# Kernel optimization log

Measured on AMD Instinct MI355X. Metric: run time of the kernel, lower is better.

The kernel has to match this reference:

```python
import jax, jax.numpy as jnp
import numpy as np

B, S, E, H = 8, 2048, 1024, 4
D = E // H  # per-head attention embed_dim (torch MHA with num_heads=1)


def setup_inputs() -> dict:
    key = jax.random.key(0)
    ks = jax.random.split(key, 7)
    scale = 0.02
    return {
        "x": jax.random.normal(ks[0], (B, S, E), dtype=jnp.float32),
        # outer linear: torch Linear(E, E) -> y = x @ W.T + b
        "W_lin": jax.random.normal(ks[1], (E, E), dtype=jnp.float32) * scale,
        "b_lin": jnp.zeros((E,), dtype=jnp.float32),
        # per-head MultiheadAttention params, stacked over H heads
        # in_proj: [3D, D] weight, [3D] bias per head (q,k,v stacked)
        "W_in": jax.random.normal(ks[2], (H, 3 * D, D), dtype=jnp.float32) * scale,
        "b_in": jnp.zeros((H, 3 * D), dtype=jnp.float32),
        # out_proj: [D, D] weight, [D] bias per head
        "W_out": jax.random.normal(ks[3], (H, D, D), dtype=jnp.float32) * scale,
        "b_out": jnp.zeros((H, D), dtype=jnp.float32),
    }


def _forward(x, W_lin, b_lin, W_in, b_in, W_out, b_out):
    # outer projection
    x_proj = jnp.einsum("bse,fe->bsf", x, W_lin) + b_lin          # [B,S,E]
    # torch.chunk(dim=-1) into H contiguous slices of width D == reshape
    xs = x_proj.reshape(B, S, H, D)                                 # [B,S,H,D]
    # per-head in_proj (q,k,v share input; weights stacked as [3D, D])
    qkv = jnp.einsum("bshd,hed->bshe", xs, W_in) + b_in             # [B,S,H,3D]
    q, k, v = jnp.split(qkv, 3, axis=-1)                            # each [B,S,H,D]
    # scaled dot-product attention per head (inner num_heads=1 -> head dim D)
    scores = jnp.einsum("bshd,bthd->bhst", q, k) / jnp.sqrt(jnp.float32(D))
    attn = jax.nn.softmax(scores, axis=-1)                          # [B,H,S,S]
    out = jnp.einsum("bhst,bthd->bshd", attn, v)                    # [B,S,H,D]
    # per-head out_proj
    out = jnp.einsum("bshd,hed->bshe", out, W_out) + b_out          # [B,S,H,D]
    # concat heads back along feature dim
    return out.reshape(B, S, E)


def reference(x, W_lin, b_lin, W_in, b_in, W_out, b_out):
    return _forward(x, W_lin, b_lin, W_in, b_in, W_out, b_out)
```

## Files before the change

### kernel.cpp

```cpp
#include <hip/hip_runtime.h>


typedef unsigned short u16;
typedef short s8v __attribute__((ext_vector_type(8)));
typedef float f4v __attribute__((ext_vector_type(4)));
typedef unsigned short us8v __attribute__((ext_vector_type(8)));

typedef const __attribute__((address_space(1))) void* gas_t;
typedef __attribute__((address_space(3))) void* las_t;

#define QSCALE 0.09016844f

__device__ __forceinline__ u16 f2bf(float f) {
  unsigned u = __builtin_bit_cast(unsigned, f);
  unsigned r = u + 0x7FFFu + ((u >> 16) & 1u);
  return (u16)(r >> 16);
}

__device__ __forceinline__ unsigned cvtpk(float a, float b) {
  unsigned r;
  asm("v_cvt_pk_bf16_f32 %0, %1, %2" : "=v"(r) : "v"(a), "v"(b));
  return r;
}

__device__ __forceinline__ void gload16(const void* g, void* l) {
  __builtin_amdgcn_global_load_lds((gas_t)g, (las_t)l, 16, 0, 0);
}

__global__ void cast_all(const float* __restrict__ x, const float* __restrict__ Wl,
                         const float* __restrict__ Wi, const float* __restrict__ Wo,
                         u16* __restrict__ xb, u16* __restrict__ WLb,
                         u16* __restrict__ WIb, u16* __restrict__ WOb) {
  const int i = blockIdx.x * blockDim.x + threadIdx.x;
  const float* src;
  u16* dst;
  int j;
  float sc = 1.0f;
  if (i < 4194304) {
    src = x; dst = xb; j = i;
  } else {
    const int k = i - 4194304;
    if (k < 262144) {
      src = Wl; dst = WLb; j = k;
    } else if (k < 458752) {
      src = Wi; dst = WIb; j = k - 262144;
      if (((j >> 6) % 768) < 256) sc = QSCALE;
    } else {
      src = Wo; dst = WOb; j = k - 458752;
    }
  }
  const float4 v = reinterpret_cast<const float4*>(src)[j];
  ushort4 o;
  o.x = f2bf(v.x * sc); o.y = f2bf(v.y * sc); o.z = f2bf(v.z * sc); o.w = f2bf(v.w * sc);
  reinterpret_cast<ushort4*>(dst)[j] = o;
}

template <int MODE>
__global__ void __launch_bounds__(256, 2) gemm128(
    const u16* __restrict__ A, const u16* __restrict__ Bw,
    const float* __restrict__ bias,
    u16* __restrict__ outB, float* __restrict__ outF,
    u16* __restrict__ Qo, u16* __restrict__ Ko, u16* __restrict__ Vo)
{
  constexpr int K    = (MODE == 0) ? 1024 : 256;
  constexpr int LDA  = 1024;
  constexpr int LDB  = (MODE == 0) ? 1024 : 256;
  constexpr int SMEM = (MODE == 1) ? 35072 : 32768;

  const int bx = blockIdx.x, ny = blockIdx.y, h = blockIdx.z;
  const int tid = threadIdx.x;
  const int wid = tid >> 6, l = tid & 63;
  const int l15 = l & 15, lg = l >> 4;
  const int wr = wid >> 1, wc = wid & 1;

  __shared__ __align__(16) char smem[SMEM];
  char* Al = smem;
  char* Bl = smem + 16384;

  const u16* Abase = A + (size_t)bx * 128 * LDA + ((MODE == 0) ? 0 : h * 256);
  const size_t bwoff = (MODE == 0) ? 0
                      : ((MODE == 1) ? (size_t)h * 768 * 256 : (size_t)h * 256 * 256);
  const u16* Bbase = Bw + bwoff + (size_t)ny * 128 * LDB;

  f4v acc[4][4];
#pragma unroll
  for (int i = 0; i < 4; ++i)
#pragma unroll
    for (int j = 0; j < 4; ++j) acc[i][j] = f4v{0.f, 0.f, 0.f, 0.f};

  for (int k0 = 0; k0 < K; k0 += 64) {
    __syncthreads();
#pragma unroll
    for (int ii = 0; ii < 4; ++ii) {
      const int i = wid * 4 + ii;
      const int row = i * 8 + (l >> 3);
      const int c = l & 7;
      gload16(Abase + (size_t)row * LDA + k0 + ((c ^ (row & 7)) << 3), Al + i * 1024);
    }
#pragma unroll
    for (int ii = 0; ii < 4; ++ii) {
      const int i = wid * 4 + ii;
      const int row = i * 8 + (l >> 3);
      const int c = l & 7;
      gload16(Bbase + (size_t)row * LDB + k0 + ((c ^ (row & 7)) << 3), Bl + i * 1024);
    }
    __syncthreads();
#pragma unroll
    for (int kf = 0; kf < 2; ++kf) {
      s8v a[4];
#pragma unroll
      for (int mf = 0; mf < 4; ++mf) {
        const int row = wr * 64 + mf * 16 + l15;
        a[mf] = *reinterpret_cast<const s8v*>(
            Al + row * 128 + (((kf * 32 + lg * 8) << 1) ^ ((row & 7) << 4)));
      }
#pragma unroll
      for (int nf = 0; nf < 4; ++nf) {
        const int n = wc * 64 + nf * 16 + l15;
        const s8v b = *reinterpret_cast<const s8v*>(
            Bl + n * 128 + (((kf * 32 + lg * 8) << 1) ^ ((n & 7) << 4)));
#pragma unroll
        for (int mf = 0; mf < 4; ++mf)
          acc[mf][nf] = __builtin_amdgcn_mfma_f32_16x16x32_bf16(a[mf], b, acc[mf][nf], 0, 0, 0);
      }
    }
  }

  const int mbase = bx * 128 + wr * 64;
  const int nbase = ny * 128 + wc * 64;

  if constexpr (MODE == 0) {
#pragma unroll
    for (int nf = 0; nf < 4; ++nf) {
      const int colg = nbase + nf * 16 + l15;
      const float bv = bias[colg];
#pragma unroll
      for (int mf = 0; mf < 4; ++mf)
#pragma unroll
        for (int r = 0; r < 4; ++r) {
          const int mr = mbase + mf * 16 + lg * 4 + r;
          outB[(size_t)mr * 1024 + colg] = f2bf(acc[mf][nf][r] + bv);
        }
    }
  } else if constexpr (MODE == 2) {
#pragma unroll
    for (int nf = 0; nf < 4; ++nf) {
      const int colg = nbase + nf * 16 + l15;
      const float bv = bias[h * 256 + colg];
#pragma unroll
      for (int mf = 0; mf < 4; ++mf)
#pragma unroll
        for (int r = 0; r < 4; ++r) {
          const int mr = mbase + mf * 16 + lg * 4 + r;
          outF[(size_t)mr * 1024 + h * 256 + colg] = acc[mf][nf][r] + bv;
        }
    }
  } else {
    if (ny < 4) {
      u16* dst = (ny < 2) ? Qo : Ko;
      const int cb = (ny < 2) ? 0 : 256;
#pragma unroll
      for (int nf = 0; nf < 4; ++nf) {
        const int colg = nbase + nf * 16 + l15;
        const float bscale = (ny < 2) ? QSCALE : 1.0f;
        const float bv = bias[h * 768 + colg] * bscale;
        const int d = colg - cb;
#pragma unroll
        for (int mf = 0; mf < 4; ++mf)
#pragma unroll
          for (int r = 0; r < 4; ++r) {
            const int mr = mbase + mf * 16 + lg * 4 + r;
            const int b = mr >> 11, s = mr & 2047;
            dst[((size_t)(b * 4 + h) * 2048 + s) * 256 + d] = f2bf(acc[mf][nf][r] + bv);
          }
      }
    } else {
      __syncthreads();
      short* tr = reinterpret_cast<short*>(smem);
#pragma unroll
      for (int nf = 0; nf < 4; ++nf) {
        const int colg = nbase + nf * 16 + l15;
        const float bv = bias[h * 768 + colg];
        const int cl = wc * 64 + nf * 16 + l15;
#pragma unroll
        for (int mf = 0; mf < 4; ++mf)
#pragma unroll
          for (int r = 0; r < 4; ++r) {
            const int rl = wr * 64 + mf * 16 + lg * 4 + r;
            tr[rl * 137 + cl] = (short)f2bf(acc[mf][nf][r] + bv);
          }
      }
      __syncthreads();
      const int b = bx >> 4;
#pragma unroll
      for (int rep = 0; rep < 8; ++rep) {
        const int u = rep * 256 + tid;
        const int d = u >> 4, sb = u & 15;
        const int dglob = (ny - 4) * 128 + d;
        const int tile = (bx & 15) * 2 + (sb >> 3);
        const int c = sb & 7;
        const int kA = 32 * (c >> 2) + 8 * ((2 * c) & 3) + 4 * ((c >> 1) & 1);
        u16* base = Vo + (((size_t)(b * 4 + h) * 32 + tile) * 256 + dglob) * 64;
        ushort4 lo, hi;
        lo.x = (u16)tr[(sb * 8 + 0) * 137 + d];
        lo.y = (u16)tr[(sb * 8 + 1) * 137 + d];
        lo.z = (u16)tr[(sb * 8 + 2) * 137 + d];
        lo.w = (u16)tr[(sb * 8 + 3) * 137 + d];
        hi.x = (u16)tr[(sb * 8 + 4) * 137 + d];
        hi.y = (u16)tr[(sb * 8 + 5) * 137 + d];
        hi.z = (u16)tr[(sb * 8 + 6) * 137 + d];
        hi.w = (u16)tr[(sb * 8 + 7) * 137 + d];
        *reinterpret_cast<ushort4*>(base + kA)     = lo;
        *reinterpret_cast<ushort4*>(base + kA + 8) = hi;
      }
    }
  }
}

__global__ void __launch_bounds__(256, 2) attn_fwd(
    const u16* __restrict__ Q, const u16* __restrict__ Kk,
    const u16* __restrict__ Vt, u16* __restrict__ AO)
{
  const int qt = blockIdx.x;
  const int bh = blockIdx.y;
  const int tid = threadIdx.x;
  const int wid = tid >> 6, l = tid & 63;
  const int l15 = l & 15, lg = l >> 4;

  __shared__ __align__(16) char smem[65536];
  char* Kl = smem;
  char* Vl = smem + 32768;

  const size_t kbase = (size_t)bh * 2048 * 256;

  s8v qa[8];
  {
    const u16* qrow = Q + ((size_t)bh * 2048 + qt * 64 + wid * 16 + l15) * 256;
#pragma unroll
    for (int kf = 0; kf < 8; ++kf)
      qa[kf] = *reinterpret_cast<const s8v*>(qrow + kf * 32 + lg * 8);
  }

  f4v O[16];
#pragma unroll
  for (int df = 0; df < 16; ++df) O[df] = f4v{0.f, 0.f, 0.f, 0.f};
  float m_run = -1e30f, l_run = 0.f;

  for (int t0 = 0; t0 < 2048; t0 += 64) {
    __syncthreads();
#pragma unroll
    for (int ii = 0; ii < 8; ++ii) {
      const int i = wid * 8 + ii;
      const int row = i * 2 + (l >> 5);
      const int c = l & 31;
      gload16(Kk + kbase + (size_t)(t0 + row) * 256 + ((c ^ (row & 7)) << 3), Kl + i * 1024);
    }
    {
      const u16* vtile = Vt + ((size_t)bh * 32 + (t0 >> 6)) * 16384;
#pragma unroll
      for (int ii = 0; ii < 8; ++ii) {
        const int i = wid * 8 + ii;
        const int d = i * 8 + (l >> 3);
        const int c = l & 7;
        gload16(vtile + (size_t)d * 64 + ((c ^ (d & 7)) << 3), Vl + i * 1024);
      }
    }
    __syncthreads();

    f4v Sx[4];
#pragma unroll
    for (int nf = 0; nf < 4; ++nf) Sx[nf] = f4v{0.f, 0.f, 0.f, 0.f};
#pragma unroll
    for (int kf = 0; kf < 8; ++kf) {
      const int ch = kf * 4 + lg;
#pragma unroll
      for (int nf = 0; nf < 4; ++nf) {
        const int tl = nf * 16 + l15;
        const s8v kb = *reinterpret_cast<const s8v*>(
            Kl + tl * 512 + ((ch ^ (tl & 7)) << 4));
        Sx[nf] = __builtin_amdgcn_mfma_f32_16x16x32_bf16(kb, qa[kf], Sx[nf], 0, 0, 0);
      }
    }

    float mloc = fmaxf(fmaxf(fmaxf(Sx[0][0], Sx[0][1]), fmaxf(Sx[0][2], Sx[0][3])),
                       fmaxf(fmaxf(Sx[1][0], Sx[1][1]), fmaxf(Sx[1][2], Sx[1][3])));
    mloc = fmaxf(mloc, fmaxf(fmaxf(Sx[2][0], Sx[2][1]), fmaxf(Sx[2][2], Sx[2][3])));
    mloc = fmaxf(mloc, fmaxf(fmaxf(Sx[3][0], Sx[3][1]), fmaxf(Sx[3][2], Sx[3][3])));
    mloc = fmaxf(mloc, __shfl_xor(mloc, 16));
    mloc = fmaxf(mloc, __shfl_xor(mloc, 32));

    if (__any(mloc > m_run + 11.5f)) {
      const float mn = fmaxf(m_run, mloc);
      const float fac = __builtin_exp2f(m_run - mn);
      m_run = mn;
      l_run *= fac;
      float facr[4];
#pragma unroll
      for (int r = 0; r < 4; ++r) facr[r] = __shfl(fac, lg * 4 + r);
#pragma unroll
      for (int df = 0; df < 16; ++df) {
        O[df][0] *= facr[0]; O[df][1] *= facr[1];
        O[df][2] *= facr[2]; O[df][3] *= facr[3];
      }
    }

    float p[4][4];
    float sum = 0.f;
#pragma unroll
    for (int nf = 0; nf < 4; ++nf)
#pragma unroll
      for (int r = 0; r < 4; ++r) {
        p[nf][r] = __builtin_exp2f(Sx[nf][r] - m_run);
        sum += p[nf][r];
      }
    sum += __shfl_xor(sum, 16);
    sum += __shfl_xor(sum, 32);
    l_run += sum;

    s8v pa[2];
#pragma unroll
    for (int kf2 = 0; kf2 < 2; ++kf2) {
      int4 w;
      w.x = (int)cvtpk(p[2 * kf2][0],     p[2 * kf2][1]);
      w.y = (int)cvtpk(p[2 * kf2][2],     p[2 * kf2][3]);
      w.z = (int)cvtpk(p[2 * kf2 + 1][0], p[2 * kf2 + 1][1]);
      w.w = (int)cvtpk(p[2 * kf2 + 1][2], p[2 * kf2 + 1][3]);
      pa[kf2] = __builtin_bit_cast(s8v, w);
    }

#pragma unroll
    for (int kf2 = 0; kf2 < 2; ++kf2) {
      const int ch = kf2 * 4 + lg;
#pragma unroll
      for (int df = 0; df < 16; ++df) {
        const int dl = df * 16 + l15;
        const s8v vb = *reinterpret_cast<const s8v*>(
            Vl + dl * 128 + ((ch ^ (dl & 7)) << 4));
        O[df] = __builtin_amdgcn_mfma_f32_16x16x32_bf16(pa[kf2], vb, O[df], 0, 0, 0);
      }
    }
  }

  const float inv = 1.0f / l_run;
  float invr[4];
#pragma unroll
  for (int r = 0; r < 4; ++r) invr[r] = __shfl(inv, lg * 4 + r);
  const int b = bh >> 2, h = bh & 3;
#pragma unroll
  for (int df = 0; df < 16; ++df)
#pragma unroll
    for (int r = 0; r < 4; ++r) {
      const int srow = qt * 64 + wid * 16 + lg * 4 + r;
      AO[(size_t)(b * 2048 + srow) * 1024 + h * 256 + df * 16 + l15] =
          f2bf(O[df][r] * invr[r]);
    }
}

extern "C" void kernel_launch(void* const* d_in, const int* in_sizes, int n_in,
                              void* d_out, int out_size, void* d_ws, size_t ws_size,
                              hipStream_t stream) {
  (void)in_sizes; (void)n_in; (void)out_size; (void)ws_size;
  const float* x     = (const float*)d_in[0];
  const float* W_lin = (const float*)d_in[1];
  const float* b_lin = (const float*)d_in[2];
  const float* W_in  = (const float*)d_in[3];
  const float* b_in  = (const float*)d_in[4];
  const float* W_out = (const float*)d_in[5];
  const float* b_out = (const float*)d_in[6];

  char* ws = (char*)d_ws;
  u16* Qb  = (u16*)(ws);
  u16* Vtb = (u16*)(ws + (32ull << 20));
  u16* AOb = (u16*)(ws + (64ull << 20));
  u16* WLb = (u16*)(ws + (96ull << 20));
  u16* WIb = (u16*)(ws + (98ull << 20));
  u16* WOb = (u16*)(ws + (98ull << 20) + 1572864ull);

  char* doc  = (char*)d_out;
  u16* xb    = (u16*)doc;
  u16* xproj = (u16*)(doc + (32ull << 20));
  u16* Kb    = (u16*)doc;
  float* outF = (float*)d_out;

  cast_all<<<18432, 256, 0, stream>>>(x, W_lin, W_in, W_out, xb, WLb, WIb, WOb);

  gemm128<0><<<dim3(128, 8, 1), 256, 0, stream>>>(xb, WLb, b_lin, xproj, nullptr,
                                                  nullptr, nullptr, nullptr);
  gemm128<1><<<dim3(128, 6, 4), 256, 0, stream>>>(xproj, WIb, b_in, nullptr, nullptr,
                                                  Qb, Kb, Vtb);
  attn_fwd<<<dim3(32, 32, 1), 256, 0, stream>>>(Qb, Kb, Vtb, AOb);
  gemm128<2><<<dim3(128, 2, 4), 256, 0, stream>>>(AOb, WOb, b_out, nullptr, outF,
                                                  nullptr, nullptr, nullptr);
}
```

Measured before the change: 325.9 us.

## Split attention waves 2x2 over query rows and key columns with LDS merge

Each wave now handles 32 query rows (two 16-row fragments) over half of each 64-key tile, rather than 16 rows over the full tile. Every K and V fragment read from LDS therefore feeds two MFMAs, roughly halving LDS read traffic per MFMA. In exchange, each wave carries two 16x256 output accumulators, which raises register pressure and may hurt occupancy at launch bounds 256,2. A final cross-wave merge of the split-key softmax state (m, l and O) through LDS adds extra syncs and shared-memory traffic.

After: 409.6 us. +25.7%, slower.

```diff
diff --git a/kernel.cpp b/kernel.cpp
--- a/kernel.cpp
+++ b/kernel.cpp
@@ -226,6 +226,8 @@
   const int tid = threadIdx.x;
   const int wid = tid >> 6, l = tid & 63;
   const int l15 = l & 15, lg = l >> 4;
+  const int qh = wid & 1;
+  const int h2 = wid >> 1;
 
   __shared__ __align__(16) char smem[65536];
   char* Kl = smem;
@@ -233,18 +235,21 @@
 
   const size_t kbase = (size_t)bh * 2048 * 256;
 
-  s8v qa[8];
-  {
-    const u16* qrow = Q + ((size_t)bh * 2048 + qt * 64 + wid * 16 + l15) * 256;
+  s8v qa[2][8];
+#pragma unroll
+  for (int mf = 0; mf < 2; ++mf) {
+    const u16* qrow = Q + ((size_t)bh * 2048 + qt * 64 + qh * 32 + mf * 16 + l15) * 256;
 #pragma unroll
     for (int kf = 0; kf < 8; ++kf)
-      qa[kf] = *reinterpret_cast<const s8v*>(qrow + kf * 32 + lg * 8);
-  }
-
-  f4v O[16];
-#pragma unroll
-  for (int df = 0; df < 16; ++df) O[df] = f4v{0.f, 0.f, 0.f, 0.f};
-  float m_run = -1e30f, l_run = 0.f;
+      qa[mf][kf] = *reinterpret_cast<const s8v*>(qrow + kf * 32 + lg * 8);
+  }
+
+  f4v O[2][16];
+#pragma unroll
+  for (int mf = 0; mf < 2; ++mf)
+#pragma unroll
+    for (int df = 0; df < 16; ++df) O[mf][df] = f4v{0.f, 0.f, 0.f, 0.f};
+  float m_run[2] = {-1e30f, -1e30f}, l_run[2] = {0.f, 0.f};
 
   for (int t0 = 0; t0 < 2048; t0 += 64) {
     __syncthreads();
@@ -267,93 +272,132 @@
     }
     __syncthreads();
 
-    f4v Sx[4];
-#pragma unroll
-    for (int nf = 0; nf < 4; ++nf) Sx[nf] = f4v{0.f, 0.f, 0.f, 0.f};
+    f4v Sx[2][2];
+#pragma unroll
+    for (int mf = 0; mf < 2; ++mf)
+#pragma unroll
+      for (int nf = 0; nf < 2; ++nf) Sx[mf][nf] = f4v{0.f, 0.f, 0.f, 0.f};
 #pragma unroll
     for (int kf = 0; kf < 8; ++kf) {
       const int ch = kf * 4 + lg;
 #pragma unroll
-      for (int nf = 0; nf < 4; ++nf) {
-        const int tl = nf * 16 + l15;
+      for (int nf = 0; nf < 2; ++nf) {
+        const int tl = h2 * 32 + nf * 16 + l15;
         const s8v kb = *reinterpret_cast<const s8v*>(
             Kl + tl * 512 + ((ch ^ (tl & 7)) << 4));
-        Sx[nf] = __builtin_amdgcn_mfma_f32_16x16x32_bf16(kb, qa[kf], Sx[nf], 0, 0, 0);
-      }
-    }
-
-    float mloc = fmaxf(fmaxf(fmaxf(Sx[0][0], Sx[0][1]), fmaxf(Sx[0][2], Sx[0][3])),
-                       fmaxf(fmaxf(Sx[1][0], Sx[1][1]), fmaxf(Sx[1][2], Sx[1][3])));
-    mloc = fmaxf(mloc, fmaxf(fmaxf(Sx[2][0], Sx[2][1]), fmaxf(Sx[2][2], Sx[2][3])));
-    mloc = fmaxf(mloc, fmaxf(fmaxf(Sx[3][0], Sx[3][1]), fmaxf(Sx[3][2], Sx[3][3])));
-    mloc = fmaxf(mloc, __shfl_xor(mloc, 16));
-    mloc = fmaxf(mloc, __shfl_xor(mloc, 32));
-
-    if (__any(mloc > m_run + 11.5f)) {
-      const float mn = fmaxf(m_run, mloc);
-      const float fac = __builtin_exp2f(m_run - mn);
-      m_run = mn;
-      l_run *= fac;
-      float facr[4];
-#pragma unroll
-      for (int r = 0; r < 4; ++r) facr[r] = __shfl(fac, lg * 4 + r);
-#pragma unroll
-      for (int df = 0; df < 16; ++df) {
-        O[df][0] *= facr[0]; O[df][1] *= facr[1];
-        O[df][2] *= facr[2]; O[df][3] *= facr[3];
-      }
-    }
-
-    float p[4][4];
-    float sum = 0.f;
-#pragma unroll
-    for (int nf = 0; nf < 4; ++nf)
-#pragma unroll
-      for (int r = 0; r < 4; ++r) {
-        p[nf][r] = __builtin_exp2f(Sx[nf][r] - m_run);
-        sum += p[nf][r];
-      }
-    sum += __shfl_xor(sum, 16);
-    sum += __shfl_xor(sum, 32);
-    l_run += sum;
+        Sx[0][nf] = __builtin_amdgcn_mfma_f32_16x16x32_bf16(kb, qa[0][kf], Sx[0][nf], 0, 0, 0);
+        Sx[1][nf] = __builtin_amdgcn_mfma_f32_16x16x32_bf16(kb, qa[1][kf], Sx[1][nf], 0, 0, 0);
+      }
+    }
 
     s8v pa[2];
 #pragma unroll
-    for (int kf2 = 0; kf2 < 2; ++kf2) {
+    for (int mf = 0; mf < 2; ++mf) {
+      float mloc = fmaxf(fmaxf(fmaxf(Sx[mf][0][0], Sx[mf][0][1]),
+                               fmaxf(Sx[mf][0][2], Sx[mf][0][3])),
+                         fmaxf(fmaxf(Sx[mf][1][0], Sx[mf][1][1]),
+                               fmaxf(Sx[mf][1][2], Sx[mf][1][3])));
+      mloc = fmaxf(mloc, __shfl_xor(mloc, 16));
+      mloc = fmaxf(mloc, __shfl_xor(mloc, 32));
+
+      if (__any(mloc > m_run[mf] + 11.5f)) {
+        const float mn = fmaxf(m_run[mf], mloc);
+        const float fac = __builtin_exp2f(m_run[mf] - mn);
+        m_run[mf] = mn;
+        l_run[mf] *= fac;
+        float facr[4];
+#pragma unroll
+        for (int r = 0; r < 4; ++r) facr[r] = __shfl(fac, lg * 4 + r);
+#pragma unroll
+        for (int df = 0; df < 16; ++df) {
+          O[mf][df][0] *= facr[0]; O[mf][df][1] *= facr[1];
+          O[mf][df][2] *= facr[2]; O[mf][df][3] *= facr[3];
+        }
+      }
+
+      float sum = 0.f;
+#pragma unroll
+      for (int nf = 0; nf < 2; ++nf)
+#pragma unroll
+        for (int r = 0; r < 4; ++r) {
+          Sx[mf][nf][r] = __builtin_exp2f(Sx[mf][nf][r] - m_run[mf]);
+          sum += Sx[mf][nf][r];
+        }
+      sum += __shfl_xor(sum, 16);
+      sum += __shfl_xor(sum, 32);
+      l_run[mf] += sum;
+
       int4 w;
-      w.x = (int)cvtpk(p[2 * kf2][0],     p[2 * kf2][1]);
-      w.y = (int)cvtpk(p[2 * kf2][2],     p[2 * kf2][3]);
-      w.z = (int)cvtpk(p[2 * kf2 + 1][0], p[2 * kf2 + 1][1]);
-      w.w = (int)cvtpk(p[2 * kf2 + 1][2], p[2 * kf2 + 1][3]);
-      pa[kf2] = __builtin_bit_cast(s8v, w);
-    }
-
-#pragma unroll
-    for (int kf2 = 0; kf2 < 2; ++kf2) {
-      const int ch = kf2 * 4 + lg;
+      w.x = (int)cvtpk(Sx[mf][0][0], Sx[mf][0][1]);
+      w.y = (int)cvtpk(Sx[mf][0][2], Sx[mf][0][3]);
+      w.z = (int)cvtpk(Sx[mf][1][0], Sx[mf][1][1]);
+      w.w = (int)cvtpk(Sx[mf][1][2], Sx[mf][1][3]);
+      pa[mf] = __builtin_bit_cast(s8v, w);
+    }
+
+    {
+      const int ch = h2 * 4 + lg;
 #pragma unroll
       for (int df = 0; df < 16; ++df) {
         const int dl = df * 16 + l15;
         const s8v vb = *reinterpret_cast<const s8v*>(
             Vl + dl * 128 + ((ch ^ (dl & 7)) << 4));
-        O[df] = __builtin_amdgcn_mfma_f32_16x16x32_bf16(pa[kf2], vb, O[df], 0, 0, 0);
-      }
-    }
-  }
-
-  const float inv = 1.0f / l_run;
-  float invr[4];
-#pragma unroll
-  for (int r = 0; r < 4; ++r) invr[r] = __shfl(inv, lg * 4 + r);
+        O[0][df] = __builtin_amdgcn_mfma_f32_16x16x32_bf16(pa[0], vb, O[0][df], 0, 0, 0);
+        O[1][df] = __builtin_amdgcn_mfma_f32_16x16x32_bf16(pa[1], vb, O[1][df], 0, 0, 0);
+      }
+    }
+  }
+
+  __syncthreads();
+  float* mlbuf = reinterpret_cast<float*>(smem);
+  float* Obuf  = reinterpret_cast<float*>(smem + 1024);
+
+  if (h2 == 1 && lg == 0) {
+    mlbuf[(qh * 2 + 0) * 16 + l15] = m_run[0];
+    mlbuf[(qh * 2 + 1) * 16 + l15] = m_run[1];
+    mlbuf[64 + (qh * 2 + 0) * 16 + l15] = l_run[0];
+    mlbuf[64 + (qh * 2 + 1) * 16 + l15] = l_run[1];
+  }
+
   const int b = bh >> 2, h = bh & 3;
 #pragma unroll
-  for (int df = 0; df < 16; ++df)
-#pragma unroll
-    for (int r = 0; r < 4; ++r) {
-      const int srow = qt * 64 + wid * 16 + lg * 4 + r;
-      AO[(size_t)(b * 2048 + srow) * 1024 + h * 256 + df * 16 + l15] =
-          f2bf(O[df][r] * invr[r]);
-    }
+  for (int mf = 0; mf < 2; ++mf) {
+    __syncthreads();
+    if (h2 == 1) {
+      float* ob = Obuf + qh * 4096;
+#pragma unroll
+      for (int df = 0; df < 16; ++df)
+#pragma unroll
+        for (int r = 0; r < 4; ++r)
+          ob[(lg * 4 + r) * 256 + df * 16 + l15] = O[mf][df][r];
+    }
+    __syncthreads();
+    if (h2 == 0) {
+      const float m0 = m_run[mf];
+      const float m1 = mlbuf[(qh * 2 + mf) * 16 + l15];
+      const float l1 = mlbuf[64 + (qh * 2 + mf) * 16 + l15];
+      const float mn = fmaxf(m0, m1);
+      const float f0 = __builtin_exp2f(m0 - mn);
+      const float f1 = __builtin_exp2f(m1 - mn);
+      const float inv = 1.0f / (l_run[mf] * f0 + l1 * f1);
+      float f0r[4], f1r[4];
+#pragma unroll
+      for (int r = 0; r < 4; ++r) {
+        f0r[r] = __shfl(f0 * inv, lg * 4 + r);
+        f1r[r] = __shfl(f1 * inv, lg * 4 + r);
+      }
+      const float* ob = Obuf + qh * 4096;
+#pragma unroll
+      for (int df = 0; df < 16; ++df)
+#pragma unroll
+        for (int r = 0; r < 4; ++r) {
+          const float v = O[mf][df][r] * f0r[r]
+                        + ob[(lg * 4 + r) * 256 + df * 16 + l15] * f1r[r];
+          const int srow = qt * 64 + qh * 32 + mf * 16 + lg * 4 + r;
+          AO[(size_t)(b * 2048 + srow) * 1024 + h * 256 + df * 16 + l15] = f2bf(v);
+        }
+    }
+  }
 }
 
 extern "C" void kernel_launch(void* const* d_in, const int* in_sizes, int n_in,
```
